# Kernel tuning notes

Measured on AMD Instinct MI355X. Metric: run time of the kernel, lower is better.

## Reference

```python
import jax, jax.numpy as jnp
from jax import lax
import numpy as np

EMBED = 20
FILTERS = 16
KSIZES = (1, 3, 5, 7, 9)
LIN_IN = 7 * len(KSIZES) * FILTERS  # 560
LIN_DIM = 64
SEQ_LENS = {'pep': 12, 'a1': 7, 'a2': 8, 'a3': 16, 'b1': 6, 'b2': 7, 'b3': 18}
BATCH = 16384


def setup_inputs() -> dict:
    key = jax.random.key(0)
    keys = jax.random.split(key, 16)
    inp = {}
    for i, (name, L) in enumerate(SEQ_LENS.items()):
        inp[name] = jax.random.normal(keys[i], (BATCH, EMBED, L), dtype=jnp.float32)
    # Conv weights: one stacked array per kernel size, [7 sequences, FILTERS, EMBED, k]
    for j, k in enumerate(KSIZES):
        inp[f'Wk{k}'] = jax.random.normal(keys[7 + j], (7, FILTERS, EMBED, k), dtype=jnp.float32) * 0.1
    inp['lin1_w'] = jax.random.normal(keys[12], (LIN_DIM, LIN_IN), dtype=jnp.float32) * 0.05
    inp['lin1_b'] = jnp.zeros((LIN_DIM,), dtype=jnp.float32)
    inp['lin2_w'] = jax.random.normal(keys[13], (1, LIN_DIM), dtype=jnp.float32) * 0.1
    inp['lin2_b'] = jnp.zeros((1,), dtype=jnp.float32)
    return inp


def _conv_relu_gmax(x, w):
    # x: [B, C, L], w: [F, C, k] -> SAME conv + ReLU + global max over length -> [B, F]
    y = lax.conv_general_dilated(x, w, window_strides=(1,), padding='SAME',
                                 dimension_numbers=('NCH', 'OIH', 'NCH'))
    return jnp.max(jax.nn.relu(y), axis=-1)


def _branch(x, ws):
    # x scaled by 1/5 as in the torch forward; concat pooled features over kernel sizes
    x = x / 5.0
    return jnp.concatenate([_conv_relu_gmax(x, w) for w in ws], axis=1)  # [B, 5*F]


def reference(pep, a1, a2, a3, b1, b2, b3, Wk1, Wk3, Wk5, Wk7, Wk9,
              lin1_w, lin1_b, lin2_w, lin2_b):
    seqs = [pep, a1, a2, a3, b1, b2, b3]
    Wks = [Wk1, Wk3, Wk5, Wk7, Wk9]
    feats = jnp.concatenate(
        [_branch(seqs[i], [W[i] for W in Wks]) for i in range(7)], axis=1)  # [B, 560]
    # Dropout is identity at inference.
    h = jax.nn.sigmoid(feats @ lin1_w.T + lin1_b)  # [B, 64]
    out = h @ lin2_w.T + lin2_b                    # [B, 1]
    return out.reshape(-1)                          # [B]
```

## Files before the change

### kernel.cpp

```cpp
#include <hip/hip_runtime.h>
#include <stdint.h>
#include <stddef.h>

typedef short bfrag __attribute__((ext_vector_type(8)));
typedef float f32x4 __attribute__((ext_vector_type(4)));
typedef float f32x4u __attribute__((ext_vector_type(4), aligned(4)));

#define NSEQ 7

__constant__ int c_ks[5] = {1, 3, 5, 7, 9};

#define SLO0 3
#define SLO1 2
#define SLO2 1
#define SLO3 0
#define SLO4 0
#define SN0 1
#define SN1 3
#define SN2 5
#define SN3 6
#define SN4 7

#define STAGE_MAX_HW 21248
#define XL_HW (STAGE_MAX_HW + 5120)

static __device__ __forceinline__ unsigned short f2bf(float f) {
  unsigned int u = __float_as_uint(f);
  u += 0x7FFFu + ((u >> 16) & 1u);
  return (unsigned short)(u >> 16);
}

struct PrepArgs {
  const float* Wk[5];
  const float* lin1_w;
  bfrag* Wpack;
  bfrag* lin1pack;
};

__global__ __launch_bounds__(256) void prep_kernel(PrepArgs a) {
  int tid = blockIdx.x * 256 + threadIdx.x;
  const int NW = NSEQ * 5 * 7 * 64;
  if (tid < NW) {
    int lane = tid & 63, rest = tid >> 6;
    int step = rest % 7, nt = (rest / 7) % 5, seq = rest / 35;
    int quad = lane >> 4, f = lane & 15;
    int ks = c_ks[nt], off = (9 - ks) >> 1;
    const float* W = a.Wk[nt];
    bfrag s;
#pragma unroll
    for (int j = 0; j < 8; ++j) {
      int k = step * 32 + quad * 8 + j;
      int t = k / 24, c = k % 24;
      int tap = t - off;
      float val = 0.f;
      if (c < 20 && tap >= 0 && tap < ks)
        val = W[((seq * 16 + f) * 20 + c) * ks + tap] * 0.2f;
      s[j] = (short)f2bf(val);
    }
    a.Wpack[tid] = s;
  } else if (tid < NW + 4 * 18 * 64) {
    int t2 = tid - NW;
    int lane = t2 & 63, rest = t2 >> 6;
    int step = rest % 18, nt = rest / 18;
    int quad = lane >> 4, col = lane & 15;
    int n = nt * 16 + col;
    bfrag s;
#pragma unroll
    for (int j = 0; j < 8; ++j) {
      int k = step * 32 + quad * 8 + j;
      float val = (k < 560) ? a.lin1_w[n * 560 + k] : 0.f;
      s[j] = (short)f2bf(val);
    }
    a.lin1pack[t2] = s;
  }
}

struct ConvArgs {
  const float* x[NSEQ];
  const bfrag* Wpack;
  unsigned short* feats;
};

template <int SLO, int SN>
static __device__ __forceinline__ void mfma_group(f32x4& acc, int s, const bfrag& Af,
                                                  const bfrag* BfBase) {
  if (s >= SLO && s < SLO + SN)
    acc = __builtin_amdgcn_mfma_f32_16x16x32_bf16(Af, BfBase[s - SLO], acc, 0, 0, 0);
}

static __device__ __forceinline__ void tile_mfma(const unsigned short* arow, const bfrag* Bf,
                                                 f32x4 acc[5]) {
#pragma unroll
  for (int s = 0; s < 7; ++s) {
    bfrag Af = *(const bfrag*)(arow + s * 32);
    mfma_group<SLO0, SN0>(acc[0], s, Af, Bf + 0);
    mfma_group<SLO1, SN1>(acc[1], s, Af, Bf + 1);
    mfma_group<SLO2, SN2>(acc[2], s, Af, Bf + 4);
    mfma_group<SLO3, SN3>(acc[3], s, Af, Bf + 9);
    acc[4] = __builtin_amdgcn_mfma_f32_16x16x32_bf16(Af, Bf[15 + s], acc[4], 0, 0, 0);
  }
}

template <int L>
__device__ __forceinline__ void conv_body(unsigned short* xl, const ConvArgs& a,
                                          const int seq, const int b0) {
  constexpr int Pv = L + 9;
  constexpr int SHW0 = Pv * 24;
  constexpr int SHW = SHW0 + ((24 - (SHW0 & 63)) & 63);
  constexpr int STAGE_HW = 32 * SHW;
  constexpr int NC = (L + 3) / 4;
  int* pmax = (int*)(xl + STAGE_MAX_HW);
  const int tid = threadIdx.x;
  const float* xg = a.x[seq];

  for (int i = tid; i < STAGE_HW / 8; i += 256) ((uint4*)xl)[i] = uint4{0, 0, 0, 0};
  for (int i = tid; i < 640; i += 256) ((uint4*)pmax)[i] = uint4{0, 0, 0, 0};
  __syncthreads();
  for (int r = tid; r < 320; r += 256) {
    int b = r / 10, cp = r - (r / 10) * 10;
    const float* rowA = xg + ((size_t)(b0 + b) * 20 + 2 * cp) * L;
    unsigned short* dst = xl + b * SHW + 4 * 24 + 2 * cp;
#pragma unroll
    for (int ci = 0; ci < NC; ++ci) {
      constexpr int dummy = 0; (void)dummy;
      int xi0 = (4 * ci > L - 4) ? (L - 4) : 4 * ci;
      f32x4u fa = *(const f32x4u*)(rowA + xi0);
      f32x4u fb = *(const f32x4u*)(rowA + L + xi0);
#pragma unroll
      for (int j = 0; j < 4; ++j) {
        unsigned int pk;
        asm("v_cvt_pk_bf16_f32 %0, %1, %2" : "=v"(pk) : "v"(fa[j]), "v"(fb[j]));
        *(unsigned int*)(dst + (xi0 + j) * 24) = pk;
      }
    }
  }
  __syncthreads();

  const int wave = tid >> 6, lane = tid & 63, quad = lane >> 4, m = lane & 15;

  const bfrag* wp = a.Wpack + (size_t)(seq * 5 * 7) * 64 + lane;
  bfrag Bf[22];
  {
    int bi = 0;
#pragma unroll
    for (int i = 0; i < SN0; ++i) Bf[bi++] = wp[(0 * 7 + SLO0 + i) * 64];
#pragma unroll
    for (int i = 0; i < SN1; ++i) Bf[bi++] = wp[(1 * 7 + SLO1 + i) * 64];
#pragma unroll
    for (int i = 0; i < SN2; ++i) Bf[bi++] = wp[(2 * 7 + SLO2 + i) * 64];
#pragma unroll
    for (int i = 0; i < SN3; ++i) Bf[bi++] = wp[(3 * 7 + SLO3 + i) * 64];
#pragma unroll
    for (int i = 0; i < SN4; ++i) Bf[bi++] = wp[(4 * 7 + SLO4 + i) * 64];
  }

#pragma unroll
  for (int mt = 0; mt < 2; ++mt) {
    f32x4 vmax[5];
#pragma unroll
    for (int g = 0; g < 5; ++g) vmax[g] = f32x4{0.f, 0.f, 0.f, 0.f};

    for (int l = wave; l < L; l += 4) {
      const unsigned short* arow = &xl[(mt * 16 + m) * SHW + l * 24 + quad * 8];
      f32x4 acc[5];
#pragma unroll
      for (int g = 0; g < 5; ++g) acc[g] = f32x4{0.f, 0.f, 0.f, 0.f};
      tile_mfma(arow, Bf, acc);
#pragma unroll
      for (int g = 0; g < 5; ++g) {
#pragma unroll
        for (int r4 = 0; r4 < 4; ++r4) vmax[g][r4] = fmaxf(vmax[g][r4], acc[g][r4]);
      }
    }

#pragma unroll
    for (int g = 0; g < 5; ++g) {
#pragma unroll
      for (int r4 = 0; r4 < 4; ++r4)
        atomicMax(&pmax[(mt * 16 + quad * 4 + r4) * 80 + g * 16 + m], __float_as_int(vmax[g][r4]));
    }
  }
  __syncthreads();

  for (int r = tid; r < 320; r += 256) {
    int s = r / 10, c = r - (r / 10) * 10;
    int k0 = seq * 80 + c * 8;
    bfrag outv;
#pragma unroll
    for (int j = 0; j < 8; ++j)
      outv[j] = (short)f2bf(__int_as_float(pmax[s * 80 + c * 8 + j]));
    int step = k0 >> 5, q = (k0 >> 3) & 3;
    int b = b0 + s;
    *(bfrag*)(a.feats + ((size_t)(b >> 4) * 18 + step) * 512 + (size_t)(q * 16 + (b & 15)) * 8) = outv;
  }
}

__global__ __launch_bounds__(256, 3) void conv_kernel(ConvArgs a) {
  __shared__ __align__(16) unsigned short xl[XL_HW];
  const int bid = blockIdx.x;
  const int seq = bid % 7;
  const int b0 = (bid / 7) * 32;
  switch (seq) {
    case 0: conv_body<12>(xl, a, 0, b0); break;
    case 1: conv_body< 7>(xl, a, 1, b0); break;
    case 2: conv_body< 8>(xl, a, 2, b0); break;
    case 3: conv_body<16>(xl, a, 3, b0); break;
    case 4: conv_body< 6>(xl, a, 4, b0); break;
    case 5: conv_body< 7>(xl, a, 5, b0); break;
    default: conv_body<18>(xl, a, 6, b0); break;
  }
}

struct MlpArgs {
  const bfrag* feats;
  const bfrag* lin1pack;
  const float* lin1_b;
  const float* lin2_w;
  const float* lin2_b;
  float* out;
};

__global__ __launch_bounds__(256, 4) void mlp_kernel(MlpArgs a) {
  __shared__ float h[16 * 68];
  __shared__ float w2[64];
  const int tid = threadIdx.x;
  const int b0 = blockIdx.x * 16;
  if (tid < 64) w2[tid] = a.lin2_w[tid];
  const int wave = tid >> 6, lane = tid & 63, quad = lane >> 4, m = lane & 15;
  const int nt = wave;
  bfrag Bf[18];
#pragma unroll
  for (int s = 0; s < 18; ++s) Bf[s] = a.lin1pack[(nt * 18 + s) * 64 + lane];
  const bfrag* ap = a.feats + (size_t)blockIdx.x * 18 * 64 + lane;
  f32x4 acc = {0.f, 0.f, 0.f, 0.f};
#pragma unroll
  for (int s = 0; s < 18; ++s)
    acc = __builtin_amdgcn_mfma_f32_16x16x32_bf16(ap[s * 64], Bf[s], acc, 0, 0, 0);
  int n = nt * 16 + m;
  float bias = a.lin1_b[n];
#pragma unroll
  for (int r = 0; r < 4; ++r) {
    float pre = acc[r] + bias;
    h[(quad * 4 + r) * 68 + n] = 1.f / (1.f + __expf(-pre));
  }
  __syncthreads();
  int bl = tid >> 4, q = tid & 15;
  const float* hr = &h[bl * 68 + q * 4];
  float s = hr[0] * w2[q * 4] + hr[1] * w2[q * 4 + 1] + hr[2] * w2[q * 4 + 2] + hr[3] * w2[q * 4 + 3];
  s += __shfl_xor(s, 1);
  s += __shfl_xor(s, 2);
  s += __shfl_xor(s, 4);
  s += __shfl_xor(s, 8);
  if (q == 0) a.out[b0 + bl] = s + a.lin2_b[0];
}

extern "C" void kernel_launch(void* const* d_in, const int* in_sizes, int n_in,
                              void* d_out, int out_size, void* d_ws, size_t ws_size,
                              hipStream_t stream) {
  (void)in_sizes; (void)n_in; (void)out_size; (void)ws_size;
  char* ws = (char*)d_ws;
  bfrag* Wpack = (bfrag*)(ws + 0);
  bfrag* lin1pack = (bfrag*)(ws + 262144);
  unsigned short* feats = (unsigned short*)(ws + 393216);

  PrepArgs pa;
  for (int j = 0; j < 5; ++j) pa.Wk[j] = (const float*)d_in[7 + j];
  pa.lin1_w = (const float*)d_in[12];
  pa.Wpack = Wpack;
  pa.lin1pack = lin1pack;
  prep_kernel<<<80, 256, 0, stream>>>(pa);

  ConvArgs ca;
  for (int i = 0; i < NSEQ; ++i) ca.x[i] = (const float*)d_in[i];
  ca.Wpack = Wpack;
  ca.feats = feats;
  conv_kernel<<<3584, 256, 0, stream>>>(ca);

  MlpArgs ma;
  ma.feats = (const bfrag*)feats;
  ma.lin1pack = lin1pack;
  ma.lin1_b = (const float*)d_in[13];
  ma.lin2_w = (const float*)d_in[14];
  ma.lin2_b = (const float*)d_in[15];
  ma.out = (float*)d_out;
  mlp_kernel<<<1024, 256, 0, stream>>>(ma);
}
```

Before: 175.6 us.

## Overlap second half-tile input loads with first half-tile MFMA compute

The staging of 32 batch rows into LDS is split into two halves of 16. The first half is loaded and converted, and the global loads for the second half are issued into registers before computing the first half-tile. They are then converted and stored to LDS before the second half-tile is computed. The per-thread work is also flattened so each thread handles one (sample, channel pair, chunk) item, giving better thread utilisation. This hides global load latency behind MFMA work, at the cost of extra registers (risking occupancy with 22 B fragments live) and one extra barrier.

```diff
diff --git a/kernel.cpp b/kernel.cpp
--- a/kernel.cpp
+++ b/kernel.cpp
@@ -109,6 +109,8 @@
   constexpr int SHW = SHW0 + ((24 - (SHW0 & 63)) & 63);
   constexpr int STAGE_HW = 32 * SHW;
   constexpr int NC = (L + 3) / 4;
+  constexpr int NJ = 160 * NC;
+  constexpr int NJA = NJ > 512 ? 512 : NJ;
   int* pmax = (int*)(xl + STAGE_MAX_HW);
   const int tid = threadIdx.x;
   const float* xg = a.x[seq];
@@ -116,25 +118,22 @@
   for (int i = tid; i < STAGE_HW / 8; i += 256) ((uint4*)xl)[i] = uint4{0, 0, 0, 0};
   for (int i = tid; i < 640; i += 256) ((uint4*)pmax)[i] = uint4{0, 0, 0, 0};
   __syncthreads();
-  for (int r = tid; r < 320; r += 256) {
-    int b = r / 10, cp = r - (r / 10) * 10;
-    const float* rowA = xg + ((size_t)(b0 + b) * 20 + 2 * cp) * L;
-    unsigned short* dst = xl + b * SHW + 4 * 24 + 2 * cp;
-#pragma unroll
-    for (int ci = 0; ci < NC; ++ci) {
-      constexpr int dummy = 0; (void)dummy;
-      int xi0 = (4 * ci > L - 4) ? (L - 4) : 4 * ci;
-      f32x4u fa = *(const f32x4u*)(rowA + xi0);
-      f32x4u fb = *(const f32x4u*)(rowA + L + xi0);
-#pragma unroll
-      for (int j = 0; j < 4; ++j) {
-        unsigned int pk;
-        asm("v_cvt_pk_bf16_f32 %0, %1, %2" : "=v"(pk) : "v"(fa[j]), "v"(fb[j]));
-        *(unsigned int*)(dst + (xi0 + j) * 24) = pk;
-      }
-    }
-  }
-  __syncthreads();
+
+  for (int j = tid; j < NJ; j += 256) {
+    int s = j / (10 * NC), r2 = j - s * (10 * NC);
+    int cp = r2 / NC, ci = r2 - cp * NC;
+    int xi0 = (4 * ci > L - 4) ? (L - 4) : 4 * ci;
+    const float* rowA = xg + ((size_t)(b0 + s) * 20 + 2 * cp) * L + xi0;
+    f32x4u fa = *(const f32x4u*)rowA;
+    f32x4u fb = *(const f32x4u*)(rowA + L);
+    unsigned short* dst = xl + s * SHW + (4 + xi0) * 24 + 2 * cp;
+#pragma unroll
+    for (int jj = 0; jj < 4; ++jj) {
+      unsigned int pk;
+      asm("v_cvt_pk_bf16_f32 %0, %1, %2" : "=v"(pk) : "v"(fa[jj]), "v"(fb[jj]));
+      *(unsigned int*)(dst + jj * 24) = pk;
+    }
+  }
 
   const int wave = tid >> 6, lane = tid & 63, quad = lane >> 4, m = lane & 15;
 
@@ -154,12 +153,34 @@
     for (int i = 0; i < SN4; ++i) Bf[bi++] = wp[(4 * 7 + SLO4 + i) * 64];
   }
 
-#pragma unroll
-  for (int mt = 0; mt < 2; ++mt) {
+  __syncthreads();
+
+  f32x4u ra0, rb0, ra1, rb1;
+  const bool v1 = (tid + 256) < NJA;
+  {
+    int j = tid;
+    int s = j / (10 * NC), r2 = j - s * (10 * NC);
+    int cp = r2 / NC, ci = r2 - cp * NC;
+    int xi0 = (4 * ci > L - 4) ? (L - 4) : 4 * ci;
+    const float* rowA = xg + ((size_t)(b0 + 16 + s) * 20 + 2 * cp) * L + xi0;
+    ra0 = *(const f32x4u*)rowA;
+    rb0 = *(const f32x4u*)(rowA + L);
+  }
+  if (v1) {
+    int j = tid + 256;
+    int s = j / (10 * NC), r2 = j - s * (10 * NC);
+    int cp = r2 / NC, ci = r2 - cp * NC;
+    int xi0 = (4 * ci > L - 4) ? (L - 4) : 4 * ci;
+    const float* rowA = xg + ((size_t)(b0 + 16 + s) * 20 + 2 * cp) * L + xi0;
+    ra1 = *(const f32x4u*)rowA;
+    rb1 = *(const f32x4u*)(rowA + L);
+  }
+  __builtin_amdgcn_sched_barrier(0);
+
+  auto compute_tile = [&](const int mt) {
     f32x4 vmax[5];
 #pragma unroll
     for (int g = 0; g < 5; ++g) vmax[g] = f32x4{0.f, 0.f, 0.f, 0.f};
-
     for (int l = wave; l < L; l += 4) {
       const unsigned short* arow = &xl[(mt * 16 + m) * SHW + l * 24 + quad * 8];
       f32x4 acc[5];
@@ -172,14 +193,65 @@
         for (int r4 = 0; r4 < 4; ++r4) vmax[g][r4] = fmaxf(vmax[g][r4], acc[g][r4]);
       }
     }
-
 #pragma unroll
     for (int g = 0; g < 5; ++g) {
 #pragma unroll
       for (int r4 = 0; r4 < 4; ++r4)
-        atomicMax(&pmax[(mt * 16 + quad * 4 + r4) * 80 + g * 16 + m], __float_as_int(vmax[g][r4]));
-    }
-  }
+        atomicMax(&pmax[(mt * 16 + quad * 4 + r4) * 80 + g * 16 + m],
+                  __float_as_int(vmax[g][r4]));
+    }
+  };
+
+  compute_tile(0);
+
+  {
+    int j = tid;
+    int s = j / (10 * NC), r2 = j - s * (10 * NC);
+    int cp = r2 / NC, ci = r2 - cp * NC;
+    int xi0 = (4 * ci > L - 4) ? (L - 4) : 4 * ci;
+    unsigned short* dst = xl + (16 + s) * SHW + (4 + xi0) * 24 + 2 * cp;
+#pragma unroll
+    for (int jj = 0; jj < 4; ++jj) {
+      unsigned int pk;
+      asm("v_cvt_pk_bf16_f32 %0, %1, %2" : "=v"(pk) : "v"(ra0[jj]), "v"(rb0[jj]));
+      *(unsigned int*)(dst + jj * 24) = pk;
+    }
+  }
+  if (v1) {
+    int j = tid + 256;
+    int s = j / (10 * NC), r2 = j - s * (10 * NC);
+    int cp = r2 / NC, ci = r2 - cp * NC;
+    int xi0 = (4 * ci > L - 4) ? (L - 4) : 4 * ci;
+    unsigned short* dst = xl + (16 + s) * SHW + (4 + xi0) * 24 + 2 * cp;
+#pragma unroll
+    for (int jj = 0; jj < 4; ++jj) {
+      unsigned int pk;
+      asm("v_cvt_pk_bf16_f32 %0, %1, %2" : "=v"(pk) : "v"(ra1[jj]), "v"(rb1[jj]));
+      *(unsigned int*)(dst + jj * 24) = pk;
+    }
+  }
+  if (NJ > NJA) {
+    for (int j = NJA + tid; j < NJ; j += 256) {
+      int s = j / (10 * NC), r2 = j - s * (10 * NC);
+      int cp = r2 / NC, ci = r2 - cp * NC;
+      int xi0 = (4 * ci > L - 4) ? (L - 4) : 4 * ci;
+      const float* rowA = xg + ((size_t)(b0 + 16 + s) * 20 + 2 * cp) * L + xi0;
+      f32x4u fa = *(const f32x4u*)rowA;
+      f32x4u fb = *(const f32x4u*)(rowA + L);
+      unsigned short* dst = xl + (16 + s) * SHW + (4 + xi0) * 24 + 2 * cp;
+#pragma unroll
+      for (int jj = 0; jj < 4; ++jj) {
+        unsigned int pk;
+        asm("v_cvt_pk_bf16_f32 %0, %1, %2" : "=v"(pk) : "v"(fa[jj]), "v"(fb[jj]));
+        *(unsigned int*)(dst + jj * 24) = pk;
+      }
+    }
+  }
+
+  __syncthreads();
+
+  compute_tile(1);
+
   __syncthreads();
 
   for (int r = tid; r < 320; r += 256) {
```

After: 181.2 us. 1.03x slower.

## Process two 32-sample chunks per conv block to amortize weight loads

Applied to the files above, without the earlier changes.

Each conv block now handles 64 batch samples in two sequential 32-sample chunks, halving the grid and reusing the register-held weight fragments and zeroed padding across chunks. The staging loop is flattened so each thread handles individual (sample, channel-pair, column) items, and the max buffer stride is padded to 84 to reduce LDS bank conflicts on atomics. This cuts per-block weight-load and setup overhead, at the cost of fewer blocks for latency hiding and a serial dependency between chunks within a block.

```diff
diff --git a/kernel.cpp b/kernel.cpp
--- a/kernel.cpp
+++ b/kernel.cpp
@@ -22,7 +22,8 @@
 #define SN4 7
 
 #define STAGE_MAX_HW 21248
-#define XL_HW (STAGE_MAX_HW + 5120)
+#define PMAX_STRIDE 84
+#define XL_HW (STAGE_MAX_HW + 32 * PMAX_STRIDE * 2)
 
 static __device__ __forceinline__ unsigned short f2bf(float f) {
   unsigned int u = __float_as_uint(f);
@@ -109,32 +110,12 @@
   constexpr int SHW = SHW0 + ((24 - (SHW0 & 63)) & 63);
   constexpr int STAGE_HW = 32 * SHW;
   constexpr int NC = (L + 3) / 4;
+  constexpr int NJ = 320 * NC;
   int* pmax = (int*)(xl + STAGE_MAX_HW);
   const int tid = threadIdx.x;
   const float* xg = a.x[seq];
 
   for (int i = tid; i < STAGE_HW / 8; i += 256) ((uint4*)xl)[i] = uint4{0, 0, 0, 0};
-  for (int i = tid; i < 640; i += 256) ((uint4*)pmax)[i] = uint4{0, 0, 0, 0};
-  __syncthreads();
-  for (int r = tid; r < 320; r += 256) {
-    int b = r / 10, cp = r - (r / 10) * 10;
-    const float* rowA = xg + ((size_t)(b0 + b) * 20 + 2 * cp) * L;
-    unsigned short* dst = xl + b * SHW + 4 * 24 + 2 * cp;
-#pragma unroll
-    for (int ci = 0; ci < NC; ++ci) {
-      constexpr int dummy = 0; (void)dummy;
-      int xi0 = (4 * ci > L - 4) ? (L - 4) : 4 * ci;
-      f32x4u fa = *(const f32x4u*)(rowA + xi0);
-      f32x4u fb = *(const f32x4u*)(rowA + L + xi0);
-#pragma unroll
-      for (int j = 0; j < 4; ++j) {
-        unsigned int pk;
-        asm("v_cvt_pk_bf16_f32 %0, %1, %2" : "=v"(pk) : "v"(fa[j]), "v"(fb[j]));
-        *(unsigned int*)(dst + (xi0 + j) * 24) = pk;
-      }
-    }
-  }
-  __syncthreads();
 
   const int wave = tid >> 6, lane = tid & 63, quad = lane >> 4, m = lane & 15;
 
@@ -154,44 +135,69 @@
     for (int i = 0; i < SN4; ++i) Bf[bi++] = wp[(4 * 7 + SLO4 + i) * 64];
   }
 
-#pragma unroll
-  for (int mt = 0; mt < 2; ++mt) {
-    f32x4 vmax[5];
-#pragma unroll
-    for (int g = 0; g < 5; ++g) vmax[g] = f32x4{0.f, 0.f, 0.f, 0.f};
-
-    for (int l = wave; l < L; l += 4) {
-      const unsigned short* arow = &xl[(mt * 16 + m) * SHW + l * 24 + quad * 8];
-      f32x4 acc[5];
-#pragma unroll
-      for (int g = 0; g < 5; ++g) acc[g] = f32x4{0.f, 0.f, 0.f, 0.f};
-      tile_mfma(arow, Bf, acc);
+  __syncthreads();
+
+#pragma unroll 1
+  for (int ch = 0; ch < 2; ++ch) {
+    const int c0 = b0 + ch * 32;
+
+    for (int i = tid; i < 32 * PMAX_STRIDE / 4; i += 256) ((uint4*)pmax)[i] = uint4{0, 0, 0, 0};
+    for (int j = tid; j < NJ; j += 256) {
+      int s = j / (10 * NC), r2 = j - s * (10 * NC);
+      int cp = r2 / NC, ci = r2 - cp * NC;
+      int xi0 = (4 * ci > L - 4) ? (L - 4) : 4 * ci;
+      const float* rowA = xg + ((size_t)(c0 + s) * 20 + 2 * cp) * L + xi0;
+      f32x4u fa = *(const f32x4u*)rowA;
+      f32x4u fb = *(const f32x4u*)(rowA + L);
+      unsigned short* dst = xl + s * SHW + (4 + xi0) * 24 + 2 * cp;
+#pragma unroll
+      for (int jj = 0; jj < 4; ++jj) {
+        unsigned int pk;
+        asm("v_cvt_pk_bf16_f32 %0, %1, %2" : "=v"(pk) : "v"(fa[jj]), "v"(fb[jj]));
+        *(unsigned int*)(dst + jj * 24) = pk;
+      }
+    }
+    __syncthreads();
+
+#pragma unroll
+    for (int mt = 0; mt < 2; ++mt) {
+      f32x4 vmax[5];
+#pragma unroll
+      for (int g = 0; g < 5; ++g) vmax[g] = f32x4{0.f, 0.f, 0.f, 0.f};
+      for (int l = wave; l < L; l += 4) {
+        const unsigned short* arow = &xl[(mt * 16 + m) * SHW + l * 24 + quad * 8];
+        f32x4 acc[5];
+#pragma unroll
+        for (int g = 0; g < 5; ++g) acc[g] = f32x4{0.f, 0.f, 0.f, 0.f};
+        tile_mfma(arow, Bf, acc);
+#pragma unroll
+        for (int g = 0; g < 5; ++g) {
+#pragma unroll
+          for (int r4 = 0; r4 < 4; ++r4) vmax[g][r4] = fmaxf(vmax[g][r4], acc[g][r4]);
+        }
+      }
 #pragma unroll
       for (int g = 0; g < 5; ++g) {
 #pragma unroll
-        for (int r4 = 0; r4 < 4; ++r4) vmax[g][r4] = fmaxf(vmax[g][r4], acc[g][r4]);
+        for (int r4 = 0; r4 < 4; ++r4)
+          atomicMax(&pmax[(mt * 16 + quad * 4 + r4) * PMAX_STRIDE + g * 16 + m],
+                    __float_as_int(vmax[g][r4]));
       }
     }
-
-#pragma unroll
-    for (int g = 0; g < 5; ++g) {
-#pragma unroll
-      for (int r4 = 0; r4 < 4; ++r4)
-        atomicMax(&pmax[(mt * 16 + quad * 4 + r4) * 80 + g * 16 + m], __float_as_int(vmax[g][r4]));
-    }
-  }
-  __syncthreads();
-
-  for (int r = tid; r < 320; r += 256) {
-    int s = r / 10, c = r - (r / 10) * 10;
-    int k0 = seq * 80 + c * 8;
-    bfrag outv;
-#pragma unroll
-    for (int j = 0; j < 8; ++j)
-      outv[j] = (short)f2bf(__int_as_float(pmax[s * 80 + c * 8 + j]));
-    int step = k0 >> 5, q = (k0 >> 3) & 3;
-    int b = b0 + s;
-    *(bfrag*)(a.feats + ((size_t)(b >> 4) * 18 + step) * 512 + (size_t)(q * 16 + (b & 15)) * 8) = outv;
+    __syncthreads();
+
+    for (int r = tid; r < 320; r += 256) {
+      int s = r / 10, c = r - (r / 10) * 10;
+      int k0 = seq * 80 + c * 8;
+      bfrag outv;
+#pragma unroll
+      for (int j = 0; j < 8; ++j)
+        outv[j] = (short)f2bf(__int_as_float(pmax[s * PMAX_STRIDE + c * 8 + j]));
+      int step = k0 >> 5, q = (k0 >> 3) & 3;
+      int b = c0 + s;
+      *(bfrag*)(a.feats + ((size_t)(b >> 4) * 18 + step) * 512 + (size_t)(q * 16 + (b & 15)) * 8) = outv;
+    }
+    if (ch == 0) __syncthreads();
   }
 }
 
@@ -199,7 +205,7 @@
   __shared__ __align__(16) unsigned short xl[XL_HW];
   const int bid = blockIdx.x;
   const int seq = bid % 7;
-  const int b0 = (bid / 7) * 32;
+  const int b0 = (bid / 7) * 64;
   switch (seq) {
     case 0: conv_body<12>(xl, a, 0, b0); break;
     case 1: conv_body< 7>(xl, a, 1, b0); break;
@@ -274,7 +280,7 @@
   for (int i = 0; i < NSEQ; ++i) ca.x[i] = (const float*)d_in[i];
   ca.Wpack = Wpack;
   ca.feats = feats;
-  conv_kernel<<<3584, 256, 0, stream>>>(ca);
+  conv_kernel<<<1792, 256, 0, stream>>>(ca);
 
   MlpArgs ma;
   ma.feats = (const bfrag*)feats;
```

New measurement: 184.1 us. 4.8% more time.
